# Kernel optimization log

Hardware: AMD Instinct MI355X
Metric: run time of the kernel (lower is better)

## Reference

```python
import jax, jax.numpy as jnp
import numpy as np

B, IN, H, N_FRAMES = 256, 1024, 2048, 32
BN_EPS = 1e-5


def setup_inputs() -> dict:
    key = jax.random.key(0)
    ks = jax.random.split(key, 10)
    s_in = 1.0 / np.sqrt(IN)
    s_h = 1.0 / np.sqrt(H)
    return {
        "x": jax.random.normal(ks[0], (B, IN), jnp.float32),
        "W_x": jax.random.normal(ks[1], (IN, 3 * H), jnp.float32) * s_in,
        "W_h": jax.random.normal(ks[2], (H, 3 * H), jnp.float32) * s_h,
        "b_x": jnp.zeros((3 * H,), jnp.float32),
        "b_h": jnp.zeros((3 * H,), jnp.float32),
        "W_d": jax.random.normal(ks[3], (H, IN), jnp.float32) * s_h,
        "b_d": jnp.zeros((IN,), jnp.float32),
        "gamma": jnp.ones((IN,), jnp.float32),
        "beta": jnp.zeros((IN,), jnp.float32),
        "n_frames": N_FRAMES,
    }


def reference(x, W_x, W_h, b_x, b_h, W_d, b_d, gamma, beta, n_frames):
    Bsz = x.shape[0]
    Hh = W_h.shape[0]
    h0 = jnp.zeros((Bsz, Hh), x.dtype)

    def step(carry, _):
        h, inp = carry
        gx = inp @ W_x + b_x                      # [B, 3H]
        gh = h @ W_h + b_h                        # [B, 3H]
        xr, xz, xn = jnp.split(gx, 3, axis=-1)
        hr, hz, hn = jnp.split(gh, 3, axis=-1)
        r = jax.nn.sigmoid(xr + hr)
        z = jax.nn.sigmoid(xz + hz)
        n = jnp.tanh(xn + r * hn)
        h_new = (1.0 - z) * n + z * h             # GRU update
        out = h_new @ W_d + b_d                   # fed back as next input
        return (h_new, out), out

    _, outs = jax.lax.scan(step, (h0, x), None, length=n_frames)  # [T, B, IN]
    # BatchNorm1d applied per frame over the batch dim (training-mode stats)
    mean = jnp.mean(outs, axis=1, keepdims=True)
    var = jnp.var(outs, axis=1, keepdims=True)
    return (outs - mean) * jax.lax.rsqrt(var + BN_EPS) * gamma + beta
```

## Files before the change

kernel.cpp:

```cpp
#include <hip/hip_runtime.h>
#include <hip/hip_bf16.h>
#include <stdint.h>


typedef __attribute__((ext_vector_type(8))) _Float16 half8;
typedef __attribute__((ext_vector_type(4))) float f32x4;
typedef __attribute__((ext_vector_type(16))) float f32x16;
typedef unsigned short u16;

#define GLB_CAST(p) ((const __attribute__((address_space(1))) void*)(p))
#define LDS_CAST(p) ((__attribute__((address_space(3))) void*)(p))

static __device__ __forceinline__ void gload_lds16(const void* g, void* l) {
  __builtin_amdgcn_global_load_lds(GLB_CAST(g), LDS_CAST(l), 16, 0, 0);
}
static __device__ __forceinline__ u16 f2h(float f) {
  _Float16 h = (_Float16)f;
  return __builtin_bit_cast(u16, h);
}
static __device__ __forceinline__ float h2f(u16 u) {
  _Float16 h = __builtin_bit_cast(_Float16, u);
  return (float)h;
}

__global__ __launch_bounds__(256) void transpose_conv(
    const float* __restrict__ src, int src_ld, int j0,
    u16* __restrict__ dst, int dst_ld)
{
  __shared__ float tile[32][33];
  const int kt = blockIdx.y * 32, jt = blockIdx.x * 32;
  const int tr = threadIdx.x >> 5, tc = threadIdx.x & 31;
#pragma unroll
  for (int r = 0; r < 4; r++)
    tile[tr + r * 8][tc] = src[(size_t)(kt + tr + r * 8) * src_ld + j0 + jt + tc];
  __syncthreads();
#pragma unroll
  for (int r = 0; r < 4; r++)
    dst[(size_t)(jt + tr + r * 8) * dst_ld + kt + tc] = f2h(tile[tc][tr + r * 8]);
}

__global__ __launch_bounds__(256) void convert_f2h(
    const float* __restrict__ src, u16* __restrict__ dst)
{
  const int i = (blockIdx.x * 256 + threadIdx.x) * 4;
  float4 v = *(const float4*)(src + i);
  dst[i + 0] = f2h(v.x); dst[i + 1] = f2h(v.y);
  dst[i + 2] = f2h(v.z); dst[i + 3] = f2h(v.w);
}

__global__ __launch_bounds__(256) void bconst_kernel(
    const float* __restrict__ bx, const float* __restrict__ bd,
    const u16* __restrict__ XT, float* __restrict__ bc)
{
  __shared__ float sbd[1024];
  const int tid = threadIdx.x;
  for (int i = tid; i < 1024; i += 256) sbd[i] = bd[i];
  __syncthreads();
  const int j = blockIdx.x * 256 + tid;
  const u16* row = XT + (size_t)j * 1024;
  float s = bx[j];
  for (int k = 0; k < 1024; k += 8) {
    half8 v = *(const half8*)(row + k);
#pragma unroll
    for (int u = 0; u < 8; u++) s += sbd[k + u] * (float)v[u];
  }
  bc[j] = s;
}

__global__ __launch_bounds__(512) void gemm_wc(
    const u16* __restrict__ A, const u16* __restrict__ Bm,
    const u16* __restrict__ HT, u16* __restrict__ Cw)
{
  __shared__ __attribute__((aligned(16))) u16 a_lds[2][128 * 64];
  __shared__ __attribute__((aligned(16))) u16 b_lds[2][128 * 64];
  const int tid = threadIdx.x, w = tid >> 6, l = tid & 63;
  const int rw = w >> 1, jw = w & 1;
  const int m0 = blockIdx.x * 128, n0 = blockIdx.y * 128;
  f32x4 acc[2][4] = {};

  const u16 *asrc[2], *bsrc[2];
#pragma unroll
  for (int rnd = 0; rnd < 2; rnd++) {
    int flat = rnd * 512 + tid;
    int row = flat >> 3, gch = (flat & 7) ^ (row & 7);
    asrc[rnd] = A + (size_t)(m0 + row) * 1024 + gch * 8;
    bsrc[rnd] = Bm + (size_t)(n0 + row) * 1024 + gch * 8;
  }
  auto stage = [&](int buf, int kk) {
#pragma unroll
    for (int rnd = 0; rnd < 2; rnd++) {
      int flat = rnd * 512 + tid;
      gload_lds16(asrc[rnd] + kk, a_lds[buf] + flat * 8);
      gload_lds16(bsrc[rnd] + kk, b_lds[buf] + flat * 8);
    }
  };
  auto compute = [&](int buf) {
    __builtin_amdgcn_s_setprio(1);
#pragma unroll
    for (int kh = 0; kh < 2; kh++) {
      const int c = kh * 4 + (l >> 4);
      half8 a[2], b[4];
#pragma unroll
      for (int mf = 0; mf < 2; mf++) {
        int arow = rw * 32 + mf * 16 + (l & 15);
        a[mf] = *(const half8*)(a_lds[buf] + (arow * 8 + (c ^ (arow & 7))) * 8);
      }
#pragma unroll
      for (int nf = 0; nf < 4; nf++) {
        int brow = jw * 64 + nf * 16 + (l & 15);
        b[nf] = *(const half8*)(b_lds[buf] + (brow * 8 + (c ^ (brow & 7))) * 8);
      }
#pragma unroll
      for (int mf = 0; mf < 2; mf++)
#pragma unroll
        for (int nf = 0; nf < 4; nf++)
          acc[mf][nf] = __builtin_amdgcn_mfma_f32_16x16x32_f16(a[mf], b[nf], acc[mf][nf], 0, 0, 0);
    }
    __builtin_amdgcn_s_setprio(0);
  };

  stage(0, 0);
#pragma unroll 1
  for (int t = 0; t < 16; ++t) {
    if (t < 15) {
      stage((t + 1) & 1, (t + 1) * 64);
      asm volatile("s_waitcnt vmcnt(4)\ns_barrier" ::: "memory");
    } else {
      asm volatile("s_waitcnt vmcnt(0)\ns_barrier" ::: "memory");
    }
    compute(t & 1);
    asm volatile("s_barrier" ::: "memory");
  }

#pragma unroll
  for (int mf = 0; mf < 2; mf++)
#pragma unroll
    for (int nf = 0; nf < 4; nf++) {
      const int n = n0 + jw * 64 + nf * 16 + (l & 15);
#pragma unroll
      for (int i = 0; i < 4; i++) {
        const int m = m0 + rw * 32 + mf * 16 + (l >> 4) * 4 + i;
        float v = acc[mf][nf][i];
        if (m < 4096) v += h2f(HT[(size_t)m * 2048 + n]);
        Cw[(size_t)m * 2048 + n] = f2h(v);
      }
    }
}

__global__ __launch_bounds__(256) void gemm_out(
    const u16* __restrict__ A, const u16* __restrict__ Bm,
    const float* __restrict__ bd, float* __restrict__ O,
    float* __restrict__ bnsum, float* __restrict__ bnsq)
{
  __shared__ __attribute__((aligned(16))) u16 a_lds[2][128 * 64];
  __shared__ __attribute__((aligned(16))) u16 b_lds[2][128 * 64];
  const int tid = threadIdx.x, w = tid >> 6, l = tid & 63;
  const int mw = w >> 1, nw = w & 1;
  const int m0 = blockIdx.x * 128, n0 = blockIdx.y * 128;
  const int lr = l & 31, lh = l >> 5;
  f32x16 acc[2][2] = {};

  const u16 *asrc[4], *bsrc[4];
#pragma unroll
  for (int rnd = 0; rnd < 4; rnd++) {
    int flat = rnd * 256 + tid;
    int row = flat >> 3, gch = (flat & 7) ^ (row & 7);
    asrc[rnd] = A + (size_t)(m0 + row) * 2048 + gch * 8;
    bsrc[rnd] = Bm + (size_t)(n0 + row) * 2048 + gch * 8;
  }
  auto stage = [&](int buf, int kk) {
#pragma unroll
    for (int rnd = 0; rnd < 4; rnd++) {
      gload_lds16(asrc[rnd] + kk, a_lds[buf] + (rnd * 256 + tid) * 8);
      gload_lds16(bsrc[rnd] + kk, b_lds[buf] + (rnd * 256 + tid) * 8);
    }
  };
  auto compute = [&](int buf) {
    __builtin_amdgcn_s_setprio(1);
#pragma unroll
    for (int ks = 0; ks < 4; ks++) {
      const int c = ks * 2 + lh;
      half8 a[2], b[2];
#pragma unroll
      for (int mf = 0; mf < 2; mf++) {
        int ar = mw * 64 + mf * 32 + lr;
        a[mf] = *(const half8*)(a_lds[buf] + (ar * 8 + (c ^ (ar & 7))) * 8);
      }
#pragma unroll
      for (int nf = 0; nf < 2; nf++) {
        int br = nw * 64 + nf * 32 + lr;
        b[nf] = *(const half8*)(b_lds[buf] + (br * 8 + (c ^ (br & 7))) * 8);
      }
#pragma unroll
      for (int mf = 0; mf < 2; mf++)
#pragma unroll
        for (int nf = 0; nf < 2; nf++)
          acc[mf][nf] = __builtin_amdgcn_mfma_f32_32x32x16_f16(a[mf], b[nf], acc[mf][nf], 0, 0, 0);
    }
    __builtin_amdgcn_s_setprio(0);
  };

  stage(0, 0);
#pragma unroll 1
  for (int t = 0; t < 32; ++t) {
    if (t < 31) {
      stage((t + 1) & 1, (t + 1) * 64);
      asm volatile("s_waitcnt vmcnt(8)\ns_barrier" ::: "memory");
    } else {
      asm volatile("s_waitcnt vmcnt(0)\ns_barrier" ::: "memory");
    }
    compute(t & 1);
    asm volatile("s_barrier" ::: "memory");
  }

  const int fr = m0 >> 8;
#pragma unroll
  for (int nf = 0; nf < 2; nf++) {
    const int n = n0 + nw * 64 + nf * 32 + lr;
    const float bb = bd[n];
    float s = 0.f, q = 0.f;
#pragma unroll
    for (int mf = 0; mf < 2; mf++)
#pragma unroll
      for (int reg = 0; reg < 16; reg++) {
        const int m = m0 + mw * 64 + mf * 32 + (reg & 3) + 8 * (reg >> 2) + 4 * lh;
        float v = acc[mf][nf][reg] + bb;
        O[(size_t)m * 1024 + n] = v;
        s += v; q += v * v;
      }
    s += __shfl_xor(s, 32, 64); q += __shfl_xor(q, 32, 64);
    if (lh == 0) {
      atomicAdd(&bnsum[fr * 1024 + n], s);
      atomicAdd(&bnsq[fr * 1024 + n], q);
    }
  }
}

__global__ __launch_bounds__(512) void frame0_kernel(
    const u16* __restrict__ x16, const u16* __restrict__ XT,
    const float* __restrict__ bx, const float* __restrict__ bh,
    float* __restrict__ h32out, u16* __restrict__ hout16)
{
  __shared__ __attribute__((aligned(16))) u16 a_lds[2][64 * 64];
  __shared__ __attribute__((aligned(16))) u16 b_lds[2][96 * 64];
  const int tid = threadIdx.x, w = tid >> 6, l = tid & 63;
  const int rw = w >> 1, jw = w & 1;
  const int jt = blockIdx.x, r0 = blockIdx.y * 64;
  f32x4 acc[3] = {};

  const int ar = tid >> 3;
  const int agch = (tid & 7) ^ (ar & 7);
  const u16* asrc = x16 + (size_t)(r0 + ar) * 1024 + agch * 8;
  const u16* bsrc0;
  const u16* bsrc1;
  {
    int row0 = tid >> 3, gch0 = (tid & 7) ^ (row0 & 7);
    bsrc0 = XT + (size_t)((row0 >> 5) * 2048 + jt * 32 + (row0 & 31)) * 1024 + gch0 * 8;
    int flat = 512 + tid;
    int row1 = flat >> 3, gch1 = (flat & 7) ^ (row1 & 7);
    bsrc1 = XT + (size_t)((row1 >> 5) * 2048 + jt * 32 + (row1 & 31)) * 1024 + gch1 * 8;
  }
  auto stage = [&](int buf, int kk) {
    gload_lds16(asrc + kk, a_lds[buf] + tid * 8);
    gload_lds16(bsrc0 + kk, b_lds[buf] + tid * 8);
    if (512 + tid < 768)
      gload_lds16(bsrc1 + kk, b_lds[buf] + (512 + tid) * 8);
  };

  stage(0, 0);
  __syncthreads();
  int cur = 0;
  for (int t = 0; t < 16; ++t) {
    if (t < 15) stage(cur ^ 1, (t + 1) * 64);
    const int arow = rw * 16 + (l & 15);
#pragma unroll
    for (int kh = 0; kh < 2; kh++) {
      int apch = (kh * 4 + (l >> 4)) ^ (arow & 7);
      half8 a = *(const half8*)(a_lds[cur] + arow * 64 + apch * 8);
#pragma unroll
      for (int s = 0; s < 3; s++) {
        int brow = s * 32 + jw * 16 + (l & 15);
        int bpch = (kh * 4 + (l >> 4)) ^ (brow & 7);
        half8 bf = *(const half8*)(b_lds[cur] + brow * 64 + bpch * 8);
        acc[s] = __builtin_amdgcn_mfma_f32_16x16x32_f16(a, bf, acc[s], 0, 0, 0);
      }
    }
    __syncthreads();
    cur ^= 1;
  }

  const int j = jt * 32 + jw * 16 + (l & 15);
  const float cR = bx[j] + bh[j];
  const float cZ = bx[2048 + j] + bh[2048 + j];
  const float cX = bx[4096 + j];
  const float hn0 = bh[4096 + j];
#pragma unroll
  for (int i = 0; i < 4; i++) {
    const int b = r0 + rw * 16 + (l >> 4) * 4 + i;
    float r = 1.f / (1.f + __expf(-(acc[0][i] + cR)));
    float z = 1.f / (1.f + __expf(-(acc[1][i] + cZ)));
    float n = tanhf(acc[2][i] + cX + r * hn0);
    float hv = (1.f - z) * n;
    h32out[b * 2048 + j] = hv;
    hout16[b * 2048 + j] = f2h(hv);
  }
}

__global__ __launch_bounds__(512) void frame_kernel(
    const u16* __restrict__ hin16,
    const u16* __restrict__ WC,
    const float* __restrict__ bc, const float* __restrict__ bh,
    const float* __restrict__ h32in, float* __restrict__ h32out,
    u16* __restrict__ hout16)
{
  __shared__ __attribute__((aligned(16))) char raw[131072];
  u16* aL = (u16*)raw;
  u16* bL = (u16*)(raw + 32768);
  float* xch = (float*)raw;
  const int tid = threadIdx.x, w = tid >> 6, l = tid & 63;
  const int cw = w & 1, kw = w >> 1;
  const int jt = blockIdx.x, r0 = blockIdx.y * 64;
  const int lr = l & 31, lh = l >> 5;

  f32x16 acc[2][2] = {};

  const u16* asrc;
  {
    int row = tid >> 3, gch = (tid & 7) ^ (row & 7);
    asrc = hin16 + (size_t)(r0 + row) * 2048 + gch * 8;
  }
  const u16* bsrc[2];
#pragma unroll
  for (int rnd = 0; rnd < 2; rnd++) {
    int flat = rnd * 512 + tid;
    int row = flat >> 3, gch = (flat & 7) ^ (row & 7);
    int sec = row >> 5, jr = row & 31;
    bsrc[rnd] = WC + (size_t)(sec * 2048 + jt * 32 + jr) * 2048 + gch * 8;
  }
  auto stage = [&](int buf, int step) {
    const int kk = step * 64;
    gload_lds16(asrc + kk, aL + buf * 4096 + tid * 8);
    gload_lds16(bsrc[0] + kk, bL + buf * 8192 + tid * 8);
    gload_lds16(bsrc[1] + kk, bL + buf * 8192 + (512 + tid) * 8);
  };
  auto compute = [&](int buf) {
    half8 a[2], b[2];
    const int c = kw * 2 + lh;
#pragma unroll
    for (int mf = 0; mf < 2; mf++) {
      int ar2 = mf * 32 + lr;
      a[mf] = *(const half8*)(aL + buf * 4096 + (ar2 * 8 + (c ^ (ar2 & 7))) * 8);
    }
#pragma unroll
    for (int nf = 0; nf < 2; nf++) {
      int br = (cw * 2 + nf) * 32 + lr;
      b[nf] = *(const half8*)(bL + buf * 8192 + (br * 8 + (c ^ (br & 7))) * 8);
    }
    __builtin_amdgcn_s_setprio(1);
#pragma unroll
    for (int mf = 0; mf < 2; mf++)
#pragma unroll
      for (int nf = 0; nf < 2; nf++)
        acc[mf][nf] = __builtin_amdgcn_mfma_f32_32x32x16_f16(a[mf], b[nf], acc[mf][nf], 0, 0, 0);
    __builtin_amdgcn_s_setprio(0);
  };

  stage(0, 0);
  stage(1, 1);
#pragma unroll 1
  for (int t = 0; t < 30; ++t) {
    stage((t + 2) & 3, t + 2);
    asm volatile("s_waitcnt vmcnt(6)\ns_barrier" ::: "memory");
    compute(t & 3);
  }
  asm volatile("s_waitcnt vmcnt(3)\ns_barrier" ::: "memory");
  compute(2);
  asm volatile("s_waitcnt vmcnt(0)\ns_barrier" ::: "memory");
  compute(3);

  __syncthreads();
#pragma unroll
  for (int mf = 0; mf < 2; mf++)
#pragma unroll
    for (int nf = 0; nf < 2; nf++)
#pragma unroll
      for (int q = 0; q < 4; q++) {
        f32x4 v;
#pragma unroll
        for (int d = 0; d < 4; d++) v[d] = acc[mf][nf][q * 4 + d];
        *(f32x4*)(xch + (cw * 4 + kw) * 4096 +
                  (((mf * 2 + nf) * 4 + q) * 64 + l) * 4) = v;
      }
  __syncthreads();

  const int mf2 = w >> 2, q2 = w & 3;
  f32x4 g[4];
#pragma unroll
  for (int sec = 0; sec < 4; sec++) {
    f32x4 s = {};
#pragma unroll
    for (int k2 = 0; k2 < 4; k2++)
      s += *(const f32x4*)(xch + ((sec >> 1) * 4 + k2) * 4096 +
                           (((mf2 * 2 + (sec & 1)) * 4 + q2) * 64 + l) * 4);
    g[sec] = s;
  }
  const int j = jt * 32 + lr;
  const float cR = bc[j] + bh[j];
  const float cZ = bc[2048 + j] + bh[2048 + j];
  const float cX = bc[4096 + j];
  const float cH = bh[4096 + j];
#pragma unroll
  for (int d = 0; d < 4; d++) {
    const int bb = r0 + mf2 * 32 + 8 * q2 + 4 * lh + d;
    float rg = 1.f / (1.f + __expf(-(g[0][d] + cR)));
    float zg = 1.f / (1.f + __expf(-(g[1][d] + cZ)));
    float ng = tanhf(g[2][d] + cX + rg * (g[3][d] + cH));
    float hp = h32in[bb * 2048 + j];
    float hv = (1.f - zg) * ng + zg * hp;
    h32out[bb * 2048 + j] = hv;
    hout16[bb * 2048 + j] = f2h(hv);
  }
}

__global__ __launch_bounds__(256) void bn_apply(
    float* __restrict__ O, const float* __restrict__ bnsum,
    const float* __restrict__ bnsq, const float* __restrict__ gamma,
    const float* __restrict__ beta)
{
  const int t = blockIdx.x, j = blockIdx.y * 256 + threadIdx.x;
  const float mean = bnsum[t * 1024 + j] * (1.f / 256.f);
  const float var = bnsq[t * 1024 + j] * (1.f / 256.f) - mean * mean;
  const float inv = rsqrtf(var + 1e-5f);
  const float g = gamma[j] * inv, be = beta[j];
  const size_t base = (size_t)t * 256 * 1024 + j;
  for (int b = 0; b < 256; b++) {
    const size_t idx = base + (size_t)b * 1024;
    O[idx] = (O[idx] - mean) * g + be;
  }
}

extern "C" void kernel_launch(void* const* d_in, const int* in_sizes, int n_in,
                              void* d_out, int out_size, void* d_ws, size_t ws_size,
                              hipStream_t stream)
{
  (void)in_sizes; (void)n_in; (void)out_size; (void)ws_size;
  const float* x  = (const float*)d_in[0];
  const float* Wx = (const float*)d_in[1];
  const float* Wh = (const float*)d_in[2];
  const float* bx = (const float*)d_in[3];
  const float* bh = (const float*)d_in[4];
  const float* Wd = (const float*)d_in[5];
  const float* bd = (const float*)d_in[6];
  const float* gamma = (const float*)d_in[7];
  const float* beta  = (const float*)d_in[8];

  char* p = (char*)d_ws;
  u16* XT  = (u16*)p;  p += (size_t)6144 * 1024 * 2;
  u16* WC  = (u16*)p;  p += (size_t)8192 * 2048 * 2;
  u16* DT  = (u16*)p;  p += (size_t)1024 * 2048 * 2;
  float* h32a = (float*)p; p += (size_t)256 * 2048 * 4;
  float* h32b = (float*)p; p += (size_t)256 * 2048 * 4;
  u16* x16 = (u16*)p;  p += (size_t)256 * 1024 * 2;
  float* bc = (float*)p; p += (size_t)6144 * 4;
  float* bnsum = (float*)p; p += (size_t)32 * 1024 * 4;
  float* bnsq  = (float*)p; p += (size_t)32 * 1024 * 4;
  u16* Hs   = (u16*)p;
  u16* HT   = (u16*)p;
  u16* Wd16 = (u16*)(p + (size_t)4096 * 2048 * 2);

  const size_t BH = (size_t)256 * 2048;

  transpose_conv<<<dim3(192, 32), 256, 0, stream>>>(Wx, 6144, 0, XT, 1024);
  transpose_conv<<<dim3(128, 64), 256, 0, stream>>>(Wh, 6144, 0, HT, 2048);
  transpose_conv<<<dim3(64, 64), 256, 0, stream>>>(Wh, 6144, 4096,
                                                   WC + (size_t)6144 * 2048, 2048);
  transpose_conv<<<dim3(32, 64), 256, 0, stream>>>(Wd, 1024, 0, DT, 2048);
  convert_f2h<<<2048, 256, 0, stream>>>(Wd, Wd16);
  convert_f2h<<<256, 256, 0, stream>>>(x, x16);
  bconst_kernel<<<24, 256, 0, stream>>>(bx, bd, XT, bc);
  hipMemsetAsync(bnsum, 0, (size_t)2 * 32 * 1024 * 4, stream);
  gemm_wc<<<dim3(48, 16), 512, 0, stream>>>(XT, Wd16, HT, WC);

  frame0_kernel<<<dim3(64, 4), 512, 0, stream>>>(x16, XT, bx, bh, h32a, Hs);
  for (int t = 1; t < 32; t++) {
    const float* hin32 = (t & 1) ? h32a : h32b;
    float* hout32      = (t & 1) ? h32b : h32a;
    frame_kernel<<<dim3(64, 4), 512, 0, stream>>>(
        Hs + (size_t)(t - 1) * BH, WC, bc, bh, hin32, hout32, Hs + (size_t)t * BH);
  }

  gemm_out<<<dim3(64, 8), 256, 0, stream>>>(Hs, DT, bd, (float*)d_out, bnsum, bnsq);
  bn_apply<<<dim3(32, 4), 256, 0, stream>>>((float*)d_out, bnsum, bnsq, gamma, beta);
}
```

Measured before the change: 699.6 us.

## Fuse recurrent frame launches into one persistent kernel with grid barrier

Replaces the 31 per-frame kernel launches with a single persistent kernel of 256 blocks that loops over time steps and synchronizes through a global atomic counter barrier. The fp32 hidden state is kept in registers across steps, so the double-buffered fp32 hidden arrays and their global reads and writes go away. This targets launch overhead and inter-kernel gaps on a latency-bound recurrence. It depends on all 256 blocks being co-resident (one per CU) to avoid deadlock, and adds spin-wait and fence costs at every step.

```diff
diff --git a/kernel.cpp b/kernel.cpp
--- a/kernel.cpp
+++ b/kernel.cpp
@@ -306,12 +306,12 @@
   }
 }
 
-__global__ __launch_bounds__(512) void frame_kernel(
-    const u16* __restrict__ hin16,
+__global__ __launch_bounds__(512) void pframe_kernel(
+    u16* __restrict__ Hs,
     const u16* __restrict__ WC,
     const float* __restrict__ bc, const float* __restrict__ bh,
-    const float* __restrict__ h32in, float* __restrict__ h32out,
-    u16* __restrict__ hout16)
+    const float* __restrict__ h32a,
+    unsigned* __restrict__ syncc)
 {
   __shared__ __attribute__((aligned(16))) char raw[131072];
   u16* aL = (u16*)raw;
@@ -319,16 +319,12 @@
   float* xch = (float*)raw;
   const int tid = threadIdx.x, w = tid >> 6, l = tid & 63;
   const int cw = w & 1, kw = w >> 1;
-  const int jt = blockIdx.x, r0 = blockIdx.y * 64;
+  const int jt = blockIdx.x & 63, r0 = (blockIdx.x >> 6) * 64;
   const int lr = l & 31, lh = l >> 5;
 
-  f32x16 acc[2][2] = {};
-
-  const u16* asrc;
-  {
-    int row = tid >> 3, gch = (tid & 7) ^ (row & 7);
-    asrc = hin16 + (size_t)(r0 + row) * 2048 + gch * 8;
-  }
+  size_t aoff;
+  { int row = tid >> 3, gch = (tid & 7) ^ (row & 7);
+    aoff = (size_t)(r0 + row) * 2048 + gch * 8; }
   const u16* bsrc[2];
 #pragma unroll
   for (int rnd = 0; rnd < 2; rnd++) {
@@ -337,88 +333,118 @@
     int sec = row >> 5, jr = row & 31;
     bsrc[rnd] = WC + (size_t)(sec * 2048 + jt * 32 + jr) * 2048 + gch * 8;
   }
-  auto stage = [&](int buf, int step) {
-    const int kk = step * 64;
-    gload_lds16(asrc + kk, aL + buf * 4096 + tid * 8);
-    gload_lds16(bsrc[0] + kk, bL + buf * 8192 + tid * 8);
-    gload_lds16(bsrc[1] + kk, bL + buf * 8192 + (512 + tid) * 8);
-  };
-  auto compute = [&](int buf) {
-    half8 a[2], b[2];
-    const int c = kw * 2 + lh;
-#pragma unroll
-    for (int mf = 0; mf < 2; mf++) {
-      int ar2 = mf * 32 + lr;
-      a[mf] = *(const half8*)(aL + buf * 4096 + (ar2 * 8 + (c ^ (ar2 & 7))) * 8);
-    }
-#pragma unroll
-    for (int nf = 0; nf < 2; nf++) {
-      int br = (cw * 2 + nf) * 32 + lr;
-      b[nf] = *(const half8*)(bL + buf * 8192 + (br * 8 + (c ^ (br & 7))) * 8);
-    }
-    __builtin_amdgcn_s_setprio(1);
-#pragma unroll
-    for (int mf = 0; mf < 2; mf++)
-#pragma unroll
-      for (int nf = 0; nf < 2; nf++)
-        acc[mf][nf] = __builtin_amdgcn_mfma_f32_32x32x16_f16(a[mf], b[nf], acc[mf][nf], 0, 0, 0);
-    __builtin_amdgcn_s_setprio(0);
-  };
-
-  stage(0, 0);
-  stage(1, 1);
-#pragma unroll 1
-  for (int t = 0; t < 30; ++t) {
-    stage((t + 2) & 3, t + 2);
-    asm volatile("s_waitcnt vmcnt(6)\ns_barrier" ::: "memory");
-    compute(t & 3);
-  }
-  asm volatile("s_waitcnt vmcnt(3)\ns_barrier" ::: "memory");
-  compute(2);
-  asm volatile("s_waitcnt vmcnt(0)\ns_barrier" ::: "memory");
-  compute(3);
-
-  __syncthreads();
-#pragma unroll
-  for (int mf = 0; mf < 2; mf++)
-#pragma unroll
-    for (int nf = 0; nf < 2; nf++)
-#pragma unroll
-      for (int q = 0; q < 4; q++) {
-        f32x4 v;
-#pragma unroll
-        for (int d = 0; d < 4; d++) v[d] = acc[mf][nf][q * 4 + d];
-        *(f32x4*)(xch + (cw * 4 + kw) * 4096 +
-                  (((mf * 2 + nf) * 4 + q) * 64 + l) * 4) = v;
-      }
-  __syncthreads();
 
   const int mf2 = w >> 2, q2 = w & 3;
-  f32x4 g[4];
-#pragma unroll
-  for (int sec = 0; sec < 4; sec++) {
-    f32x4 s = {};
-#pragma unroll
-    for (int k2 = 0; k2 < 4; k2++)
-      s += *(const f32x4*)(xch + ((sec >> 1) * 4 + k2) * 4096 +
-                           (((mf2 * 2 + (sec & 1)) * 4 + q2) * 64 + l) * 4);
-    g[sec] = s;
-  }
   const int j = jt * 32 + lr;
   const float cR = bc[j] + bh[j];
   const float cZ = bc[2048 + j] + bh[2048 + j];
   const float cX = bc[4096 + j];
   const float cH = bh[4096 + j];
+  float hprev[4];
 #pragma unroll
   for (int d = 0; d < 4; d++) {
     const int bb = r0 + mf2 * 32 + 8 * q2 + 4 * lh + d;
-    float rg = 1.f / (1.f + __expf(-(g[0][d] + cR)));
-    float zg = 1.f / (1.f + __expf(-(g[1][d] + cZ)));
-    float ng = tanhf(g[2][d] + cX + rg * (g[3][d] + cH));
-    float hp = h32in[bb * 2048 + j];
-    float hv = (1.f - zg) * ng + zg * hp;
-    h32out[bb * 2048 + j] = hv;
-    hout16[bb * 2048 + j] = f2h(hv);
+    hprev[d] = h32a[bb * 2048 + j];
+  }
+
+#pragma unroll 1
+  for (int t = 1; t < 32; ++t) {
+    const u16* asrc = Hs + (size_t)(t - 1) * 524288 + aoff;
+    u16* hout16 = Hs + (size_t)t * 524288;
+
+    f32x16 acc[2][2] = {};
+
+    auto stage = [&](int buf, int step) {
+      const int kk = step * 64;
+      gload_lds16(asrc + kk, aL + buf * 4096 + tid * 8);
+      gload_lds16(bsrc[0] + kk, bL + buf * 8192 + tid * 8);
+      gload_lds16(bsrc[1] + kk, bL + buf * 8192 + (512 + tid) * 8);
+    };
+    auto compute = [&](int buf) {
+      half8 a[2], b[2];
+      const int c = kw * 2 + lh;
+#pragma unroll
+      for (int mf = 0; mf < 2; mf++) {
+        int ar2 = mf * 32 + lr;
+        a[mf] = *(const half8*)(aL + buf * 4096 + (ar2 * 8 + (c ^ (ar2 & 7))) * 8);
+      }
+#pragma unroll
+      for (int nf = 0; nf < 2; nf++) {
+        int br = (cw * 2 + nf) * 32 + lr;
+        b[nf] = *(const half8*)(bL + buf * 8192 + (br * 8 + (c ^ (br & 7))) * 8);
+      }
+      __builtin_amdgcn_s_setprio(1);
+#pragma unroll
+      for (int mf = 0; mf < 2; mf++)
+#pragma unroll
+        for (int nf = 0; nf < 2; nf++)
+          acc[mf][nf] = __builtin_amdgcn_mfma_f32_32x32x16_f16(a[mf], b[nf], acc[mf][nf], 0, 0, 0);
+      __builtin_amdgcn_s_setprio(0);
+    };
+
+    stage(0, 0);
+    stage(1, 1);
+#pragma unroll 1
+    for (int s = 0; s < 30; ++s) {
+      stage((s + 2) & 3, s + 2);
+      asm volatile("s_waitcnt vmcnt(6)\ns_barrier" ::: "memory");
+      compute(s & 3);
+    }
+    asm volatile("s_waitcnt vmcnt(3)\ns_barrier" ::: "memory");
+    compute(2);
+    asm volatile("s_waitcnt vmcnt(0)\ns_barrier" ::: "memory");
+    compute(3);
+
+    __syncthreads();
+#pragma unroll
+    for (int mf = 0; mf < 2; mf++)
+#pragma unroll
+      for (int nf = 0; nf < 2; nf++)
+#pragma unroll
+        for (int q = 0; q < 4; q++) {
+          f32x4 v;
+#pragma unroll
+          for (int d = 0; d < 4; d++) v[d] = acc[mf][nf][q * 4 + d];
+          *(f32x4*)(xch + (cw * 4 + kw) * 4096 +
+                    (((mf * 2 + nf) * 4 + q) * 64 + l) * 4) = v;
+        }
+    __syncthreads();
+
+    f32x4 g[4];
+#pragma unroll
+    for (int sec = 0; sec < 4; sec++) {
+      f32x4 s2 = {};
+#pragma unroll
+      for (int k2 = 0; k2 < 4; k2++)
+        s2 += *(const f32x4*)(xch + ((sec >> 1) * 4 + k2) * 4096 +
+                              (((mf2 * 2 + (sec & 1)) * 4 + q2) * 64 + l) * 4);
+      g[sec] = s2;
+    }
+#pragma unroll
+    for (int d = 0; d < 4; d++) {
+      const int bb = r0 + mf2 * 32 + 8 * q2 + 4 * lh + d;
+      float rg = 1.f / (1.f + __expf(-(g[0][d] + cR)));
+      float zg = 1.f / (1.f + __expf(-(g[1][d] + cZ)));
+      float ng = tanhf(g[2][d] + cX + rg * (g[3][d] + cH));
+      float hv = (1.f - zg) * ng + zg * hprev[d];
+      hprev[d] = hv;
+      hout16[bb * 2048 + j] = f2h(hv);
+    }
+
+    if (t < 31) {
+      __syncthreads();
+      if (tid == 0) {
+        __builtin_amdgcn_fence(__ATOMIC_RELEASE, "agent");
+        __hip_atomic_fetch_add(syncc, 1u, __ATOMIC_RELAXED,
+                               __HIP_MEMORY_SCOPE_AGENT);
+        const unsigned tgt = 256u * (unsigned)t;
+        while (__hip_atomic_load(syncc, __ATOMIC_RELAXED,
+                                 __HIP_MEMORY_SCOPE_AGENT) < tgt)
+          __builtin_amdgcn_s_sleep(2);
+        __builtin_amdgcn_fence(__ATOMIC_ACQUIRE, "agent");
+      }
+      __syncthreads();
+    }
   }
 }
 
@@ -459,16 +485,14 @@
   u16* WC  = (u16*)p;  p += (size_t)8192 * 2048 * 2;
   u16* DT  = (u16*)p;  p += (size_t)1024 * 2048 * 2;
   float* h32a = (float*)p; p += (size_t)256 * 2048 * 4;
-  float* h32b = (float*)p; p += (size_t)256 * 2048 * 4;
   u16* x16 = (u16*)p;  p += (size_t)256 * 1024 * 2;
   float* bc = (float*)p; p += (size_t)6144 * 4;
   float* bnsum = (float*)p; p += (size_t)32 * 1024 * 4;
   float* bnsq  = (float*)p; p += (size_t)32 * 1024 * 4;
+  unsigned* syncc = (unsigned*)p; p += 256;
   u16* Hs   = (u16*)p;
   u16* HT   = (u16*)p;
   u16* Wd16 = (u16*)(p + (size_t)4096 * 2048 * 2);
-
-  const size_t BH = (size_t)256 * 2048;
 
   transpose_conv<<<dim3(192, 32), 256, 0, stream>>>(Wx, 6144, 0, XT, 1024);
   transpose_conv<<<dim3(128, 64), 256, 0, stream>>>(Wh, 6144, 0, HT, 2048);
@@ -478,16 +502,11 @@
   convert_f2h<<<2048, 256, 0, stream>>>(Wd, Wd16);
   convert_f2h<<<256, 256, 0, stream>>>(x, x16);
   bconst_kernel<<<24, 256, 0, stream>>>(bx, bd, XT, bc);
-  hipMemsetAsync(bnsum, 0, (size_t)2 * 32 * 1024 * 4, stream);
+  hipMemsetAsync(bnsum, 0, (size_t)2 * 32 * 1024 * 4 + 256, stream);
   gemm_wc<<<dim3(48, 16), 512, 0, stream>>>(XT, Wd16, HT, WC);
 
   frame0_kernel<<<dim3(64, 4), 512, 0, stream>>>(x16, XT, bx, bh, h32a, Hs);
-  for (int t = 1; t < 32; t++) {
-    const float* hin32 = (t & 1) ? h32a : h32b;
-    float* hout32      = (t & 1) ? h32b : h32a;
-    frame_kernel<<<dim3(64, 4), 512, 0, stream>>>(
-        Hs + (size_t)(t - 1) * BH, WC, bc, bh, hin32, hout32, Hs + (size_t)t * BH);
-  }
+  pframe_kernel<<<256, 512, 0, stream>>>(Hs, WC, bc, bh, h32a, syncc);
 
   gemm_out<<<dim3(64, 8), 256, 0, stream>>>(Hs, DT, bd, (float*)d_out, bnsum, bnsq);
   bn_apply<<<dim3(32, 4), 256, 0, stream>>>((float*)d_out, bnsum, bnsq, gamma, beta);
```

Result: slower. 906.0 us (+29.5%).

## Halve frame kernel row tile to launch twice as many smaller blocks

Applied to the files above, without the earlier changes.

The per-frame recurrent GEMM kernel now processes 32 batch rows per block with 256 threads instead of 64 rows with 512 threads. The grid doubles from 256 to 512 blocks, LDS use drops from 128KB to 80KB, and the wave split, cross-wave reduction and epilogue indexing are rewritten to match. The goal is to fill more of the GPU's compute units on this latency-bound sequential loop, at the cost of loading each weight tile twice as often and less weight reuse per block.

```diff
diff --git a/kernel.cpp b/kernel.cpp
--- a/kernel.cpp
+++ b/kernel.cpp
@@ -306,62 +306,57 @@
   }
 }
 
-__global__ __launch_bounds__(512) void frame_kernel(
+__global__ __launch_bounds__(256) void frame_kernel(
     const u16* __restrict__ hin16,
     const u16* __restrict__ WC,
     const float* __restrict__ bc, const float* __restrict__ bh,
     const float* __restrict__ h32in, float* __restrict__ h32out,
     u16* __restrict__ hout16)
 {
-  __shared__ __attribute__((aligned(16))) char raw[131072];
+  __shared__ __attribute__((aligned(16))) char raw[81920];
   u16* aL = (u16*)raw;
-  u16* bL = (u16*)(raw + 32768);
+  u16* bL = (u16*)(raw + 16384);
   float* xch = (float*)raw;
   const int tid = threadIdx.x, w = tid >> 6, l = tid & 63;
   const int cw = w & 1, kw = w >> 1;
-  const int jt = blockIdx.x, r0 = blockIdx.y * 64;
+  const int jt = blockIdx.x, r0 = blockIdx.y * 32;
   const int lr = l & 31, lh = l >> 5;
 
-  f32x16 acc[2][2] = {};
+  f32x16 acc[2] = {};
 
   const u16* asrc;
   {
     int row = tid >> 3, gch = (tid & 7) ^ (row & 7);
     asrc = hin16 + (size_t)(r0 + row) * 2048 + gch * 8;
   }
-  const u16* bsrc[2];
-#pragma unroll
-  for (int rnd = 0; rnd < 2; rnd++) {
-    int flat = rnd * 512 + tid;
+  const u16* bsrc[4];
+#pragma unroll
+  for (int rnd = 0; rnd < 4; rnd++) {
+    int flat = rnd * 256 + tid;
     int row = flat >> 3, gch = (flat & 7) ^ (row & 7);
     int sec = row >> 5, jr = row & 31;
     bsrc[rnd] = WC + (size_t)(sec * 2048 + jt * 32 + jr) * 2048 + gch * 8;
   }
   auto stage = [&](int buf, int step) {
     const int kk = step * 64;
-    gload_lds16(asrc + kk, aL + buf * 4096 + tid * 8);
-    gload_lds16(bsrc[0] + kk, bL + buf * 8192 + tid * 8);
-    gload_lds16(bsrc[1] + kk, bL + buf * 8192 + (512 + tid) * 8);
+    gload_lds16(asrc + kk, aL + buf * 2048 + tid * 8);
+#pragma unroll
+    for (int rnd = 0; rnd < 4; rnd++)
+      gload_lds16(bsrc[rnd] + kk, bL + buf * 8192 + (rnd * 256 + tid) * 8);
   };
   auto compute = [&](int buf) {
-    half8 a[2], b[2];
-    const int c = kw * 2 + lh;
-#pragma unroll
-    for (int mf = 0; mf < 2; mf++) {
-      int ar2 = mf * 32 + lr;
-      a[mf] = *(const half8*)(aL + buf * 4096 + (ar2 * 8 + (c ^ (ar2 & 7))) * 8);
-    }
-#pragma unroll
-    for (int nf = 0; nf < 2; nf++) {
-      int br = (cw * 2 + nf) * 32 + lr;
-      b[nf] = *(const half8*)(bL + buf * 8192 + (br * 8 + (c ^ (br & 7))) * 8);
-    }
     __builtin_amdgcn_s_setprio(1);
 #pragma unroll
-    for (int mf = 0; mf < 2; mf++)
-#pragma unroll
-      for (int nf = 0; nf < 2; nf++)
-        acc[mf][nf] = __builtin_amdgcn_mfma_f32_32x32x16_f16(a[mf], b[nf], acc[mf][nf], 0, 0, 0);
+    for (int ks = 0; ks < 2; ks++) {
+      const int c = (kw * 2 + ks) * 2 + lh;
+      half8 a = *(const half8*)(aL + buf * 2048 + (lr * 8 + (c ^ (lr & 7))) * 8);
+#pragma unroll
+      for (int nf = 0; nf < 2; nf++) {
+        int br = (cw * 2 + nf) * 32 + lr;
+        half8 b = *(const half8*)(bL + buf * 8192 + (br * 8 + (c ^ (br & 7))) * 8);
+        acc[nf] = __builtin_amdgcn_mfma_f32_32x32x16_f16(a, b, acc[nf], 0, 0, 0);
+      }
+    }
     __builtin_amdgcn_s_setprio(0);
   };
 
@@ -370,38 +365,34 @@
 #pragma unroll 1
   for (int t = 0; t < 30; ++t) {
     stage((t + 2) & 3, t + 2);
-    asm volatile("s_waitcnt vmcnt(6)\ns_barrier" ::: "memory");
+    asm volatile("s_waitcnt vmcnt(10)\ns_barrier" ::: "memory");
     compute(t & 3);
   }
-  asm volatile("s_waitcnt vmcnt(3)\ns_barrier" ::: "memory");
+  asm volatile("s_waitcnt vmcnt(5)\ns_barrier" ::: "memory");
   compute(2);
   asm volatile("s_waitcnt vmcnt(0)\ns_barrier" ::: "memory");
   compute(3);
 
   __syncthreads();
 #pragma unroll
-  for (int mf = 0; mf < 2; mf++)
-#pragma unroll
-    for (int nf = 0; nf < 2; nf++)
-#pragma unroll
-      for (int q = 0; q < 4; q++) {
-        f32x4 v;
-#pragma unroll
-        for (int d = 0; d < 4; d++) v[d] = acc[mf][nf][q * 4 + d];
-        *(f32x4*)(xch + (cw * 4 + kw) * 4096 +
-                  (((mf * 2 + nf) * 4 + q) * 64 + l) * 4) = v;
-      }
+  for (int nf = 0; nf < 2; nf++)
+#pragma unroll
+    for (int q = 0; q < 4; q++) {
+      f32x4 v;
+#pragma unroll
+      for (int d = 0; d < 4; d++) v[d] = acc[nf][q * 4 + d];
+      *(f32x4*)(xch + (cw * 2 + kw) * 2048 + (nf * 4 + q) * 256 + l * 4) = v;
+    }
   __syncthreads();
 
-  const int mf2 = w >> 2, q2 = w & 3;
   f32x4 g[4];
 #pragma unroll
   for (int sec = 0; sec < 4; sec++) {
     f32x4 s = {};
 #pragma unroll
-    for (int k2 = 0; k2 < 4; k2++)
-      s += *(const f32x4*)(xch + ((sec >> 1) * 4 + k2) * 4096 +
-                           (((mf2 * 2 + (sec & 1)) * 4 + q2) * 64 + l) * 4);
+    for (int k2 = 0; k2 < 2; k2++)
+      s += *(const f32x4*)(xch + ((sec >> 1) * 2 + k2) * 2048 +
+                           ((sec & 1) * 4 + w) * 256 + l * 4);
     g[sec] = s;
   }
   const int j = jt * 32 + lr;
@@ -411,7 +402,7 @@
   const float cH = bh[4096 + j];
 #pragma unroll
   for (int d = 0; d < 4; d++) {
-    const int bb = r0 + mf2 * 32 + 8 * q2 + 4 * lh + d;
+    const int bb = r0 + 8 * w + 4 * lh + d;
     float rg = 1.f / (1.f + __expf(-(g[0][d] + cR)));
     float zg = 1.f / (1.f + __expf(-(g[1][d] + cZ)));
     float ng = tanhf(g[2][d] + cX + rg * (g[3][d] + cH));
@@ -485,7 +476,7 @@
   for (int t = 1; t < 32; t++) {
     const float* hin32 = (t & 1) ? h32a : h32b;
     float* hout32      = (t & 1) ? h32b : h32a;
-    frame_kernel<<<dim3(64, 4), 512, 0, stream>>>(
+    frame_kernel<<<dim3(64, 8), 256, 0, stream>>>(
         Hs + (size_t)(t - 1) * BH, WC, bc, bh, hin32, hout32, Hs + (size_t)t * BH);
   }
 
```

New measurement: 796.3 us. 1.14x slower.
